# Optimization experiments

Hardware: AMD Instinct MI355X
Metric: run time of the kernel (lower is better)

The kernel has to match this reference:

```python
import jax, jax.numpy as jnp
import numpy as np

N, D, H, E, K = 4096, 512, 2048, 8, 2  # tokens, input_size, hidden_size, num_experts, top_k


def setup_inputs() -> dict:
    key = jax.random.key(0)
    ks = jax.random.split(key, 4)
    x = jax.random.normal(ks[0], (N, D), dtype=jnp.float32)
    # torch init: weights ~ N(0, 0.001), biases zero
    Wg = jax.random.normal(ks[1], (D, E), dtype=jnp.float32) * 0.001
    bg = jnp.zeros((E,), jnp.float32)
    W1 = jax.random.normal(ks[2], (E, D, H), dtype=jnp.float32) * 0.001
    b1 = jnp.zeros((E, H), jnp.float32)
    W2 = jax.random.normal(ks[3], (E, H, D), dtype=jnp.float32) * 0.001
    b2 = jnp.zeros((E, D), jnp.float32)
    return {"x": x, "Wg": Wg, "bg": bg, "W1": W1, "b1": b1, "W2": W2, "b2": b2}


def reference(x, Wg, bg, W1, b1, W2, b2):
    # Gating: softmax over experts
    gates = jax.nn.softmax(x @ Wg + bg, axis=-1)            # [N, E]
    top_w, top_i = jax.lax.top_k(gates, K)                  # [N, K]
    top_w = top_w / jnp.sum(top_w, axis=-1, keepdims=True)  # renormalize

    # Expert MLP (fc1 -> fc2, no nonlinearity per source). Vectorized across all
    # experts, then gather the top-k selected outputs per token.
    h1 = jnp.einsum('nd,edh->neh', x, W1) + b1              # [N, E, H]
    all_out = jnp.einsum('neh,ehd->ned', h1, W2) + b2       # [N, E, D]
    sel = jnp.take_along_axis(all_out, top_i[:, :, None], axis=1)  # [N, K, D]

    combined = jnp.einsum('nkd,nk->nd', sel, top_w)         # [N, D]

    # usage counts: scatter-add of (detached) top-k weights per expert
    usage = jnp.zeros((E,), x.dtype).at[top_i.reshape(-1)].add(
        jax.lax.stop_gradient(top_w).reshape(-1))
    return combined, usage
```

## Files before the change

### kernel.cpp

```cpp
#include <hip/hip_runtime.h>
#include <hip/hip_bf16.h>


#define N_TOK 4096
#define DIM   512
#define HID   2048
#define NEXP  8
#define TOTSLOT (2 * N_TOK)
#define MAXTILE 72

typedef __attribute__((ext_vector_type(8))) short short8;
typedef __attribute__((ext_vector_type(4))) float f32x4;

static __device__ __forceinline__ unsigned short f2bf(float f) {
    __hip_bfloat16 b = __float2bfloat16(f);
    return *reinterpret_cast<unsigned short*>(&b);
}
static __device__ __forceinline__ float bf2f(unsigned short u) {
    return __uint_as_float((unsigned)u << 16);
}

static __device__ __forceinline__ void load16_to_lds(const void* g, void* l) {
    __builtin_amdgcn_global_load_lds(
        (const __attribute__((address_space(1))) unsigned int*)g,
        (__attribute__((address_space(3))) unsigned int*)l, 16, 0, 0);
}

__global__ __launch_bounds__(256) void gating_kernel(
    const float* __restrict__ x, const float* __restrict__ Wg,
    const float* __restrict__ bg,
    int* __restrict__ cnt, int* __restrict__ te, float* __restrict__ tw,
    float* __restrict__ usage, unsigned short* __restrict__ Xb)
{
    __shared__ int   lcnt[NEXP];
    __shared__ float lus[NEXP];
    int tid = threadIdx.x;
    if (tid < NEXP) { lcnt[tid] = 0; lus[tid] = 0.f; }
    __syncthreads();

    int wave = tid >> 6;
    int lane = tid & 63;

    for (int t = 0; t < 4; ++t) {
        int n = blockIdx.x * 16 + wave * 4 + t;

        float acc[NEXP];
#pragma unroll
        for (int e = 0; e < NEXP; ++e) acc[e] = 0.f;

#pragma unroll
        for (int it = 0; it < DIM / 64; ++it) {
            int d = it * 64 + lane;
            float xv = x[n * DIM + d];
            Xb[n * DIM + d] = f2bf(xv);
            float4 wa = *(const float4*)&Wg[d * NEXP];
            float4 wb = *(const float4*)&Wg[d * NEXP + 4];
            acc[0] += xv * wa.x; acc[1] += xv * wa.y;
            acc[2] += xv * wa.z; acc[3] += xv * wa.w;
            acc[4] += xv * wb.x; acc[5] += xv * wb.y;
            acc[6] += xv * wb.z; acc[7] += xv * wb.w;
        }
#pragma unroll
        for (int m = 32; m >= 1; m >>= 1) {
#pragma unroll
            for (int e = 0; e < NEXP; ++e)
                acc[e] += __shfl_xor(acc[e], m, 64);
        }
        if (lane == 0) {
            float l[NEXP];
#pragma unroll
            for (int e = 0; e < NEXP; ++e) l[e] = acc[e] + bg[e];
            int i0 = 0;
#pragma unroll
            for (int e = 1; e < NEXP; ++e) if (l[e] > l[i0]) i0 = e;
            int i1 = (i0 == 0) ? 1 : 0;
#pragma unroll
            for (int e = 0; e < NEXP; ++e)
                if (e != i0 && l[e] > l[i1]) i1 = e;
            float w0 = 1.f / (1.f + expf(l[i1] - l[i0]));
            float w1 = 1.f - w0;
            te[n * 2] = i0; te[n * 2 + 1] = i1;
            tw[n * 2] = w0; tw[n * 2 + 1] = w1;
            atomicAdd(&lcnt[i0], 1);
            atomicAdd(&lcnt[i1], 1);
            atomicAdd(&lus[i0], w0);
            atomicAdd(&lus[i1], w1);
        }
    }
    __syncthreads();
    if (tid < NEXP) {
        if (lcnt[tid]) atomicAdd(&cnt[tid], lcnt[tid]);
        if (lus[tid] != 0.f) atomicAdd(&usage[tid], lus[tid]);
    }
}

__global__ void prefix_kernel(const int* __restrict__ cnt,
                              int* __restrict__ offs, int* __restrict__ fill,
                              unsigned short* __restrict__ tile_tab,
                              int* __restrict__ ntile)
{
    if (threadIdx.x == 0) {
        int s = 0, nt = 0;
        for (int e = 0; e < NEXP; ++e) {
            offs[e] = s; s += cnt[e];
            int t = (cnt[e] + 127) >> 7;
            for (int i = 0; i < t; ++i)
                tile_tab[nt++] = (unsigned short)((e << 8) | i);
        }
        *ntile = nt;
        for (int i = nt; i < MAXTILE; ++i) tile_tab[i] = 0;
    }
    if (threadIdx.x < NEXP) fill[threadIdx.x] = 0;
}

__global__ __launch_bounds__(256) void scatter_kernel(
    int* __restrict__ te, const float* __restrict__ tw,
    const int* __restrict__ offs, int* __restrict__ fill,
    int* __restrict__ btok, float* __restrict__ bwt)
{
    __shared__ int lcnt[NEXP];
    __shared__ int gbase[NEXP];
    int tid = threadIdx.x;
    if (tid < NEXP) lcnt[tid] = 0;
    __syncthreads();
    int n = blockIdx.x * 256 + tid;
    int e0 = te[n * 2], e1 = te[n * 2 + 1];
    int l0 = atomicAdd(&lcnt[e0], 1);
    int l1 = atomicAdd(&lcnt[e1], 1);
    __syncthreads();
    if (tid < NEXP) gbase[tid] = atomicAdd(&fill[tid], lcnt[tid]);
    __syncthreads();
    int s0 = offs[e0] + gbase[e0] + l0;
    int s1 = offs[e1] + gbase[e1] + l1;
    btok[s0] = n; bwt[s0] = tw[n * 2];
    btok[s1] = n; bwt[s1] = tw[n * 2 + 1];
    te[n * 2] = s0; te[n * 2 + 1] = s1;
}

__global__ __launch_bounds__(256) void transpose_cvt_kernel(
    const float* __restrict__ in, unsigned short* __restrict__ out,
    int R, int C)
{
    __shared__ unsigned short tile[64][65];
    int e = blockIdx.z;
    const float* src = in + (size_t)e * R * C;
    unsigned short* dst = out + (size_t)e * R * C;
    int r0 = blockIdx.x * 64, c0 = blockIdx.y * 64;
    int tid = threadIdx.x;
    int rr = tid >> 2, cb = (tid & 3) * 16;
#pragma unroll
    for (int i = 0; i < 4; ++i) {
        float4 v = *(const float4*)&src[(size_t)(r0 + rr) * C + c0 + cb + i * 4];
        tile[rr][cb + i * 4 + 0] = f2bf(v.x);
        tile[rr][cb + i * 4 + 1] = f2bf(v.y);
        tile[rr][cb + i * 4 + 2] = f2bf(v.z);
        tile[rr][cb + i * 4 + 3] = f2bf(v.w);
    }
    __syncthreads();
#pragma unroll
    for (int i = 0; i < 4; ++i) {
        ushort4 u;
        u.x = tile[cb + i * 4 + 0][rr];
        u.y = tile[cb + i * 4 + 1][rr];
        u.z = tile[cb + i * 4 + 2][rr];
        u.w = tile[cb + i * 4 + 3][rr];
        *(ushort4*)&dst[(size_t)(c0 + rr) * R + r0 + cb + i * 4] = u;
    }
}


__global__ __launch_bounds__(256) void gemm1_kernel(
    const unsigned short* __restrict__ Xb, const unsigned short* __restrict__ W1t,
    const float* __restrict__ b1, const int* __restrict__ cnt,
    const int* __restrict__ offs, const int* __restrict__ btok,
    const unsigned short* __restrict__ tile_tab, const int* __restrict__ ntile,
    unsigned short* __restrict__ H1)
{
    __shared__ __align__(16) unsigned short Ws[128 * 64];
    __shared__ __align__(16) unsigned short Xs[128 * 64];
    __shared__ int tok_s[128];

    int ti = blockIdx.x;
    if (ti >= *ntile) return;
    unsigned short tv = tile_tab[ti];
    int e = tv >> 8, tt = tv & 255, ht = blockIdx.y;
    int cn = cnt[e];
    int off_e = offs[e];
    int tid = threadIdx.x;

    if (tid < 128) {
        int lr = tt * 128 + tid;
        tok_s[tid] = (lr < cn) ? btok[off_e + lr] : 0;
    }
    __syncthreads();

    int wave = tid >> 6, lane = tid & 63;
    int mbase = (wave >> 1) * 64, nbase = (wave & 1) * 64;
    int quad = lane >> 4, lcol = lane & 15;
    f32x4 acc[4][4];
#pragma unroll
    for (int mi = 0; mi < 4; ++mi)
#pragma unroll
        for (int ni = 0; ni < 4; ++ni)
            acc[mi][ni] = (f32x4){0.f, 0.f, 0.f, 0.f};

    int Rb = tid >> 3, pc = tid & 7;
    const unsigned short* Wsrc = W1t + ((size_t)e * HID + ht * 128) * DIM;

    for (int k0 = 0; k0 < DIM; k0 += 64) {
#pragma unroll
        for (int p = 0; p < 4; ++p) {
            int R = Rb + p * 32;
            int c = pc ^ (R & 7);
            load16_to_lds(&Wsrc[(size_t)R * DIM + k0 + c * 8], &Ws[R * 64 + pc * 8]);
            load16_to_lds(&Xb[(size_t)tok_s[R] * DIM + k0 + c * 8], &Xs[R * 64 + pc * 8]);
        }
        __syncthreads();
#pragma unroll
        for (int h = 0; h < 2; ++h) {
            int cs = ((h * 4 + quad) ^ (lcol & 7)) * 8;
            short8 a[4], b[4];
#pragma unroll
            for (int i = 0; i < 4; ++i) {
                a[i] = *(const short8*)&Ws[(mbase + i * 16 + lcol) * 64 + cs];
                b[i] = *(const short8*)&Xs[(nbase + i * 16 + lcol) * 64 + cs];
            }
#pragma unroll
            for (int mi = 0; mi < 4; ++mi)
#pragma unroll
                for (int ni = 0; ni < 4; ++ni)
                    acc[mi][ni] = __builtin_amdgcn_mfma_f32_16x16x32_bf16(
                        a[mi], b[ni], acc[mi][ni], 0, 0, 0);
        }
        __syncthreads();
    }

    float4 bv[4];
#pragma unroll
    for (int mi = 0; mi < 4; ++mi)
        bv[mi] = *(const float4*)&b1[e * HID + ht * 128 + mbase + mi * 16 + quad * 4];
#pragma unroll
    for (int ni = 0; ni < 4; ++ni) {
        int tn = tt * 128 + nbase + ni * 16 + lcol;
        if (tn >= cn) continue;
        size_t srow = (size_t)(off_e + tn) * HID + ht * 128;
#pragma unroll
        for (int mi = 0; mi < 4; ++mi) {
            int hh = mbase + mi * 16 + quad * 4;
            ushort4 u;
            u.x = f2bf(acc[mi][ni][0] + bv[mi].x);
            u.y = f2bf(acc[mi][ni][1] + bv[mi].y);
            u.z = f2bf(acc[mi][ni][2] + bv[mi].z);
            u.w = f2bf(acc[mi][ni][3] + bv[mi].w);
            *(ushort4*)&H1[srow + hh] = u;
        }
    }
}

#define KSPLIT 2
#define KCH (HID / KSPLIT)

__global__ __launch_bounds__(256) void gemm2_kernel(
    const unsigned short* __restrict__ H1, const unsigned short* __restrict__ W2t,
    const float* __restrict__ b2, const int* __restrict__ cnt,
    const int* __restrict__ offs, const int* __restrict__ btok,
    const float* __restrict__ bwt,
    const unsigned short* __restrict__ tile_tab, const int* __restrict__ ntile,
    unsigned short* __restrict__ O)
{
    __shared__ __align__(16) unsigned short Ws[128 * 64];
    __shared__ __align__(16) unsigned short Hs[128 * 64];
    __shared__ float wt_s[128];

    int ti = blockIdx.x;
    if (ti >= *ntile) return;
    unsigned short tv = tile_tab[ti];
    int e = tv >> 8, tt = tv & 255, dt = blockIdx.y, kz = blockIdx.z;
    int cn = cnt[e];
    int off_e = offs[e];
    int sb = off_e + tt * 128;
    int tid = threadIdx.x;

    if (tid < 128) {
        int lr = tt * 128 + tid;
        wt_s[tid] = (lr < cn) ? bwt[off_e + lr] : 0.f;
    }
    __syncthreads();

    int wave = tid >> 6, lane = tid & 63;
    int mbase = (wave >> 1) * 64, nbase = (wave & 1) * 64;
    int quad = lane >> 4, lcol = lane & 15;
    f32x4 acc[4][4];
#pragma unroll
    for (int mi = 0; mi < 4; ++mi)
#pragma unroll
        for (int ni = 0; ni < 4; ++ni)
            acc[mi][ni] = (f32x4){0.f, 0.f, 0.f, 0.f};

    int Rb = tid >> 3, pc = tid & 7;
    const unsigned short* Wsrc = W2t + ((size_t)e * DIM + dt * 128) * HID;

    for (int k0 = kz * KCH; k0 < (kz + 1) * KCH; k0 += 64) {
#pragma unroll
        for (int p = 0; p < 4; ++p) {
            int R = Rb + p * 32;
            int c = pc ^ (R & 7);
            int sr = sb + R; if (sr > TOTSLOT - 1) sr = TOTSLOT - 1;
            load16_to_lds(&Wsrc[(size_t)R * HID + k0 + c * 8], &Ws[R * 64 + pc * 8]);
            load16_to_lds(&H1[(size_t)sr * HID + k0 + c * 8], &Hs[R * 64 + pc * 8]);
        }
        __syncthreads();
#pragma unroll
        for (int h = 0; h < 2; ++h) {
            int cs = ((h * 4 + quad) ^ (lcol & 7)) * 8;
            short8 a[4], b[4];
#pragma unroll
            for (int i = 0; i < 4; ++i) {
                a[i] = *(const short8*)&Hs[(mbase + i * 16 + lcol) * 64 + cs];
                b[i] = *(const short8*)&Ws[(nbase + i * 16 + lcol) * 64 + cs];
            }
#pragma unroll
            for (int mi = 0; mi < 4; ++mi)
#pragma unroll
                for (int ni = 0; ni < 4; ++ni)
                    acc[mi][ni] = __builtin_amdgcn_mfma_f32_16x16x32_bf16(
                        a[mi], b[ni], acc[mi][ni], 0, 0, 0);
        }
        __syncthreads();
    }

    unsigned short* Oe = O + ((size_t)kz * TOTSLOT + sb) * DIM + dt * 128;
#pragma unroll
    for (int ni = 0; ni < 4; ++ni) {
        int dl = nbase + ni * 16 + lcol;
        float bv = (kz == 0) ? b2[e * DIM + dt * 128 + dl] : 0.f;
#pragma unroll
        for (int mi = 0; mi < 4; ++mi) {
            int rl = mbase + mi * 16 + quad * 4;
#pragma unroll
            for (int r = 0; r < 4; ++r) {
                int sl = rl + r;
                if (tt * 128 + sl < cn)
                    Oe[(size_t)sl * DIM + dl] = f2bf(wt_s[sl] * (acc[mi][ni][r] + bv));
            }
        }
    }
}

__global__ __launch_bounds__(256) void combine_kernel(
    const unsigned short* __restrict__ O, const int* __restrict__ sidx,
    float* __restrict__ out)
{
    int tid = threadIdx.x;
    int n = blockIdx.x * 2 + (tid >> 7);
    int dd = (tid & 127) * 4;
    int s0 = sidx[n * 2], s1 = sidx[n * 2 + 1];
    ushort4 a = *(const ushort4*)&O[(size_t)s0 * DIM + dd];
    ushort4 b = *(const ushort4*)&O[((size_t)TOTSLOT + s0) * DIM + dd];
    ushort4 c = *(const ushort4*)&O[(size_t)s1 * DIM + dd];
    ushort4 d = *(const ushort4*)&O[((size_t)TOTSLOT + s1) * DIM + dd];
    float4 o;
    o.x = bf2f(a.x) + bf2f(b.x) + bf2f(c.x) + bf2f(d.x);
    o.y = bf2f(a.y) + bf2f(b.y) + bf2f(c.y) + bf2f(d.y);
    o.z = bf2f(a.z) + bf2f(b.z) + bf2f(c.z) + bf2f(d.z);
    o.w = bf2f(a.w) + bf2f(b.w) + bf2f(c.w) + bf2f(d.w);
    *(float4*)&out[(size_t)n * DIM + dd] = o;
}

#define TN 16
#define HC 256
#define NCHUNK (HID / HC)

__global__ __launch_bounds__(256) void gating_fb_kernel(
    const float* __restrict__ x, const float* __restrict__ Wg,
    const float* __restrict__ bg,
    int* __restrict__ cnt, int* __restrict__ btok, float* __restrict__ bwt,
    float* __restrict__ usage)
{
    int wave = threadIdx.x >> 6;
    int lane = threadIdx.x & 63;
    int n = blockIdx.x * 4 + wave;
    float acc[NEXP];
#pragma unroll
    for (int e = 0; e < NEXP; ++e) acc[e] = 0.f;
    for (int d = lane; d < DIM; d += 64) {
        float xv = x[n * DIM + d];
        float4 wa = *(const float4*)&Wg[d * NEXP];
        float4 wb = *(const float4*)&Wg[d * NEXP + 4];
        acc[0] += xv * wa.x; acc[1] += xv * wa.y;
        acc[2] += xv * wa.z; acc[3] += xv * wa.w;
        acc[4] += xv * wb.x; acc[5] += xv * wb.y;
        acc[6] += xv * wb.z; acc[7] += xv * wb.w;
    }
#pragma unroll
    for (int m = 32; m >= 1; m >>= 1)
#pragma unroll
        for (int e = 0; e < NEXP; ++e)
            acc[e] += __shfl_xor(acc[e], m, 64);
    if (lane == 0) {
        float l[NEXP];
#pragma unroll
        for (int e = 0; e < NEXP; ++e) l[e] = acc[e] + bg[e];
        int i0 = 0;
#pragma unroll
        for (int e = 1; e < NEXP; ++e) if (l[e] > l[i0]) i0 = e;
        int i1 = (i0 == 0) ? 1 : 0;
#pragma unroll
        for (int e = 0; e < NEXP; ++e)
            if (e != i0 && l[e] > l[i1]) i1 = e;
        float w0 = 1.f / (1.f + expf(l[i1] - l[i0]));
        float w1 = 1.f - w0;
        int p0 = atomicAdd(&cnt[i0], 1);
        btok[i0 * N_TOK + p0] = n; bwt[i0 * N_TOK + p0] = w0;
        int p1 = atomicAdd(&cnt[i1], 1);
        btok[i1 * N_TOK + p1] = n; bwt[i1 * N_TOK + p1] = w1;
        atomicAdd(&usage[i0], w0);
        atomicAdd(&usage[i1], w1);
    }
}

__global__ __launch_bounds__(256) void expert_fb_kernel(
    const float* __restrict__ x, const float* __restrict__ W1,
    const float* __restrict__ b1, const float* __restrict__ W2,
    const float* __restrict__ b2, const int* __restrict__ cnt,
    const int* __restrict__ btok, const float* __restrict__ bwt,
    float* __restrict__ out)
{
    __shared__ float xs[TN][DIM];
    __shared__ float h1s[TN][HC];
    __shared__ int   tok_s[TN];
    __shared__ float wt_s[TN];
    int e = blockIdx.x >> 8;
    int tile = blockIdx.x & 255;
    int cn = cnt[e];
    int n0 = tile * TN;
    if (n0 >= cn) return;
    int nt = min(TN, cn - n0);
    int tid = threadIdx.x;
    if (tid < TN) {
        if (tid < nt) { tok_s[tid] = btok[e * N_TOK + n0 + tid]; wt_s[tid] = bwt[e * N_TOK + n0 + tid]; }
        else          { tok_s[tid] = 0; wt_s[tid] = 0.f; }
    }
    __syncthreads();
    for (int idx = tid; idx < TN * DIM; idx += 256) {
        int t = idx >> 9, d = idx & 511;
        xs[t][d] = (t < nt) ? x[tok_s[t] * DIM + d] : 0.f;
    }
    const float* W1e = W1 + (size_t)e * DIM * HID;
    const float* W2e = W2 + (size_t)e * HID * DIM;
    int tg = tid >> 6, lane = tid & 63;
    float oacc[4][8];
    {
        float4 ba = *(const float4*)&b2[e * DIM + lane * 8];
        float4 bb = *(const float4*)&b2[e * DIM + lane * 8 + 4];
#pragma unroll
        for (int ti = 0; ti < 4; ++ti) {
            oacc[ti][0] = ba.x; oacc[ti][1] = ba.y; oacc[ti][2] = ba.z; oacc[ti][3] = ba.w;
            oacc[ti][4] = bb.x; oacc[ti][5] = bb.y; oacc[ti][6] = bb.z; oacc[ti][7] = bb.w;
        }
    }
    __syncthreads();
    for (int ch = 0; ch < NCHUNK; ++ch) {
        int h0 = ch * HC;
        float f[4][4];
        {
            float4 b1v = *(const float4*)&b1[e * HID + h0 + lane * 4];
#pragma unroll
            for (int ti = 0; ti < 4; ++ti) {
                f[ti][0] = b1v.x; f[ti][1] = b1v.y; f[ti][2] = b1v.z; f[ti][3] = b1v.w;
            }
        }
        for (int d = 0; d < DIM; ++d) {
            float4 w1v = *(const float4*)&W1e[(size_t)d * HID + h0 + lane * 4];
#pragma unroll
            for (int ti = 0; ti < 4; ++ti) {
                float xv = xs[tg + 4 * ti][d];
                f[ti][0] += xv * w1v.x; f[ti][1] += xv * w1v.y;
                f[ti][2] += xv * w1v.z; f[ti][3] += xv * w1v.w;
            }
        }
        __syncthreads();
#pragma unroll
        for (int ti = 0; ti < 4; ++ti)
            *(float4*)&h1s[tg + 4 * ti][lane * 4] = make_float4(f[ti][0], f[ti][1], f[ti][2], f[ti][3]);
        __syncthreads();
        for (int j = 0; j < HC; ++j) {
            const float* w2row = &W2e[(size_t)(h0 + j) * DIM + lane * 8];
            float4 wa = *(const float4*)w2row;
            float4 wb = *(const float4*)(w2row + 4);
#pragma unroll
            for (int ti = 0; ti < 4; ++ti) {
                float hv = h1s[tg + 4 * ti][j];
                oacc[ti][0] += hv * wa.x; oacc[ti][1] += hv * wa.y;
                oacc[ti][2] += hv * wa.z; oacc[ti][3] += hv * wa.w;
                oacc[ti][4] += hv * wb.x; oacc[ti][5] += hv * wb.y;
                oacc[ti][6] += hv * wb.z; oacc[ti][7] += hv * wb.w;
            }
        }
    }
#pragma unroll
    for (int ti = 0; ti < 4; ++ti) {
        int t = tg + 4 * ti;
        if (t < nt) {
            float w = wt_s[t];
            float* o = &out[(size_t)tok_s[t] * DIM + lane * 8];
#pragma unroll
            for (int c = 0; c < 8; ++c)
                atomicAdd(&o[c], w * oacc[ti][c]);
        }
    }
}

extern "C" void kernel_launch(void* const* d_in, const int* in_sizes, int n_in,
                              void* d_out, int out_size, void* d_ws, size_t ws_size,
                              hipStream_t stream) {
    const float* x  = (const float*)d_in[0];
    const float* Wg = (const float*)d_in[1];
    const float* bg = (const float*)d_in[2];
    const float* W1 = (const float*)d_in[3];
    const float* b1 = (const float*)d_in[4];
    const float* W2 = (const float*)d_in[5];
    const float* b2 = (const float*)d_in[6];

    float* out   = (float*)d_out;
    float* usage = out + (size_t)N_TOK * DIM;

    char* ws = (char*)d_ws;
    int*   cnt  = (int*)(ws + 0);
    int*   fill = (int*)(ws + 32);
    int*   offs = (int*)(ws + 64);
    unsigned short* tile_tab = (unsigned short*)(ws + 96);
    int*   ntile = (int*)(ws + 240);
    int*   te   = (int*)(ws + 256);
    float* tw   = (float*)(ws + 33024);
    int*   btok = (int*)(ws + 65792);
    float* bwt  = (float*)(ws + 98560);
    unsigned short* Xb  = (unsigned short*)(ws + 131328);
    unsigned short* W1t = (unsigned short*)(ws + 4325632);
    unsigned short* O   = W1t;
    unsigned short* W2t = (unsigned short*)(ws + 21102848);
    unsigned short* H1  = (unsigned short*)(ws + 37880064);
    const size_t WS_NEED = 71434496ULL;

    if (ws_size >= WS_NEED) {
        hipMemsetAsync(cnt, 0, 32, stream);
        hipMemsetAsync(usage, 0, NEXP * sizeof(float), stream);
        transpose_cvt_kernel<<<dim3(DIM / 64, HID / 64, NEXP), 256, 0, stream>>>(W1, W1t, DIM, HID);
        transpose_cvt_kernel<<<dim3(HID / 64, DIM / 64, NEXP), 256, 0, stream>>>(W2, W2t, HID, DIM);
        gating_kernel<<<N_TOK / 16, 256, 0, stream>>>(x, Wg, bg, cnt, te, tw, usage, Xb);
        prefix_kernel<<<1, 64, 0, stream>>>(cnt, offs, fill, tile_tab, ntile);
        scatter_kernel<<<N_TOK / 256, 256, 0, stream>>>(te, tw, offs, fill, btok, bwt);
        gemm1_kernel<<<dim3(MAXTILE, HID / 128), 256, 0, stream>>>(
            Xb, W1t, b1, cnt, offs, btok, tile_tab, ntile, H1);
        gemm2_kernel<<<dim3(MAXTILE, DIM / 128, KSPLIT), 256, 0, stream>>>(
            H1, W2t, b2, cnt, offs, btok, bwt, tile_tab, ntile, O);
        combine_kernel<<<N_TOK / 2, 256, 0, stream>>>(O, te, out);
    } else {
        int*   fcnt  = (int*)d_ws;
        int*   fbtok = (int*)((char*)d_ws + 256);
        float* fbwt  = (float*)((char*)d_ws + 256 + (size_t)NEXP * N_TOK * sizeof(int));
        hipMemsetAsync(d_out, 0, (size_t)(N_TOK * DIM + NEXP) * sizeof(float), stream);
        hipMemsetAsync(d_ws, 0, 256, stream);
        gating_fb_kernel<<<N_TOK / 4, 256, 0, stream>>>(x, Wg, bg, fcnt, fbtok, fbwt, usage);
        expert_fb_kernel<<<NEXP * (N_TOK / TN), 256, 0, stream>>>(
            x, W1, b1, W2, b2, fcnt, fbtok, fbwt, out);
    }
}
```

Baseline: 224.7 us.

## Double-buffer LDS tiles in both expert GEMMs and remap tile block order

```diff
diff --git a/kernel.cpp b/kernel.cpp
--- a/kernel.cpp
+++ b/kernel.cpp
@@ -176,11 +176,12 @@
     const unsigned short* __restrict__ tile_tab, const int* __restrict__ ntile,
     unsigned short* __restrict__ H1)
 {
-    __shared__ __align__(16) unsigned short Ws[128 * 64];
-    __shared__ __align__(16) unsigned short Xs[128 * 64];
+    __shared__ __align__(16) unsigned short Ws[2][128 * 64];
+    __shared__ __align__(16) unsigned short Xs[2][128 * 64];
     __shared__ int tok_s[128];
 
-    int ti = blockIdx.x;
+    int bx = blockIdx.x;
+    int ti = (bx & 7) * (MAXTILE / 8) + (bx >> 3);
     if (ti >= *ntile) return;
     unsigned short tv = tile_tab[ti];
     int e = tv >> 8, tt = tv & 255, ht = blockIdx.y;
@@ -207,23 +208,31 @@
     int Rb = tid >> 3, pc = tid & 7;
     const unsigned short* Wsrc = W1t + ((size_t)e * HID + ht * 128) * DIM;
 
-    for (int k0 = 0; k0 < DIM; k0 += 64) {
+    auto stage = [&](int buf, int k0) {
 #pragma unroll
         for (int p = 0; p < 4; ++p) {
             int R = Rb + p * 32;
             int c = pc ^ (R & 7);
-            load16_to_lds(&Wsrc[(size_t)R * DIM + k0 + c * 8], &Ws[R * 64 + pc * 8]);
-            load16_to_lds(&Xb[(size_t)tok_s[R] * DIM + k0 + c * 8], &Xs[R * 64 + pc * 8]);
-        }
-        __syncthreads();
+            load16_to_lds(&Wsrc[(size_t)R * DIM + k0 + c * 8], &Ws[buf][R * 64 + pc * 8]);
+            load16_to_lds(&Xb[(size_t)tok_s[R] * DIM + k0 + c * 8], &Xs[buf][R * 64 + pc * 8]);
+        }
+    };
+
+    stage(0, 0);
+    __syncthreads();
+
+    const int NT = DIM / 64;
+    for (int t = 0; t < NT; ++t) {
+        int cur = t & 1;
+        if (t + 1 < NT) stage(cur ^ 1, (t + 1) * 64);
 #pragma unroll
         for (int h = 0; h < 2; ++h) {
             int cs = ((h * 4 + quad) ^ (lcol & 7)) * 8;
             short8 a[4], b[4];
 #pragma unroll
             for (int i = 0; i < 4; ++i) {
-                a[i] = *(const short8*)&Ws[(mbase + i * 16 + lcol) * 64 + cs];
-                b[i] = *(const short8*)&Xs[(nbase + i * 16 + lcol) * 64 + cs];
+                a[i] = *(const short8*)&Ws[cur][(mbase + i * 16 + lcol) * 64 + cs];
+                b[i] = *(const short8*)&Xs[cur][(nbase + i * 16 + lcol) * 64 + cs];
             }
 #pragma unroll
             for (int mi = 0; mi < 4; ++mi)
@@ -268,11 +277,12 @@
     const unsigned short* __restrict__ tile_tab, const int* __restrict__ ntile,
     unsigned short* __restrict__ O)
 {
-    __shared__ __align__(16) unsigned short Ws[128 * 64];
-    __shared__ __align__(16) unsigned short Hs[128 * 64];
+    __shared__ __align__(16) unsigned short Ws[2][128 * 64];
+    __shared__ __align__(16) unsigned short Hs[2][128 * 64];
     __shared__ float wt_s[128];
 
-    int ti = blockIdx.x;
+    int bx = blockIdx.x;
+    int ti = (bx & 7) * (MAXTILE / 8) + (bx >> 3);
     if (ti >= *ntile) return;
     unsigned short tv = tile_tab[ti];
     int e = tv >> 8, tt = tv & 255, dt = blockIdx.y, kz = blockIdx.z;
@@ -300,24 +310,32 @@
     int Rb = tid >> 3, pc = tid & 7;
     const unsigned short* Wsrc = W2t + ((size_t)e * DIM + dt * 128) * HID;
 
-    for (int k0 = kz * KCH; k0 < (kz + 1) * KCH; k0 += 64) {
+    auto stage = [&](int buf, int k0) {
 #pragma unroll
         for (int p = 0; p < 4; ++p) {
             int R = Rb + p * 32;
             int c = pc ^ (R & 7);
             int sr = sb + R; if (sr > TOTSLOT - 1) sr = TOTSLOT - 1;
-            load16_to_lds(&Wsrc[(size_t)R * HID + k0 + c * 8], &Ws[R * 64 + pc * 8]);
-            load16_to_lds(&H1[(size_t)sr * HID + k0 + c * 8], &Hs[R * 64 + pc * 8]);
-        }
-        __syncthreads();
+            load16_to_lds(&Wsrc[(size_t)R * HID + k0 + c * 8], &Ws[buf][R * 64 + pc * 8]);
+            load16_to_lds(&H1[(size_t)sr * HID + k0 + c * 8], &Hs[buf][R * 64 + pc * 8]);
+        }
+    };
+
+    stage(0, kz * KCH);
+    __syncthreads();
+
+    const int NT = KCH / 64;
+    for (int t = 0; t < NT; ++t) {
+        int cur = t & 1;
+        if (t + 1 < NT) stage(cur ^ 1, kz * KCH + (t + 1) * 64);
 #pragma unroll
         for (int h = 0; h < 2; ++h) {
             int cs = ((h * 4 + quad) ^ (lcol & 7)) * 8;
             short8 a[4], b[4];
 #pragma unroll
             for (int i = 0; i < 4; ++i) {
-                a[i] = *(const short8*)&Hs[(mbase + i * 16 + lcol) * 64 + cs];
-                b[i] = *(const short8*)&Ws[(nbase + i * 16 + lcol) * 64 + cs];
+                a[i] = *(const short8*)&Hs[cur][(mbase + i * 16 + lcol) * 64 + cs];
+                b[i] = *(const short8*)&Ws[cur][(nbase + i * 16 + lcol) * 64 + cs];
             }
 #pragma unroll
             for (int mi = 0; mi < 4; ++mi)
```

Result: slower. 239.6 us (+6.6%).

## Halve gemm2 token tile and swizzle expert tiles across XCDs

Applied to the files above, without the earlier changes.

```diff
diff --git a/kernel.cpp b/kernel.cpp
--- a/kernel.cpp
+++ b/kernel.cpp
@@ -7,7 +7,8 @@
 #define HID   2048
 #define NEXP  8
 #define TOTSLOT (2 * N_TOK)
-#define MAXTILE 72
+#define M1TILE 72
+#define M2TILE 144
 
 typedef __attribute__((ext_vector_type(8))) short short8;
 typedef __attribute__((ext_vector_type(4))) float f32x4;
@@ -96,19 +97,18 @@
 
 __global__ void prefix_kernel(const int* __restrict__ cnt,
                               int* __restrict__ offs, int* __restrict__ fill,
-                              unsigned short* __restrict__ tile_tab,
+                              int* __restrict__ tb128, int* __restrict__ tb64,
                               int* __restrict__ ntile)
 {
     if (threadIdx.x == 0) {
-        int s = 0, nt = 0;
+        int s = 0, a = 0, b = 0;
         for (int e = 0; e < NEXP; ++e) {
             offs[e] = s; s += cnt[e];
-            int t = (cnt[e] + 127) >> 7;
-            for (int i = 0; i < t; ++i)
-                tile_tab[nt++] = (unsigned short)((e << 8) | i);
-        }
-        *ntile = nt;
-        for (int i = nt; i < MAXTILE; ++i) tile_tab[i] = 0;
+            tb128[e] = a; a += (cnt[e] + 127) >> 7;
+            tb64[e]  = b; b += (cnt[e] + 63) >> 6;
+        }
+        tb128[NEXP] = a; tb64[NEXP] = b;
+        ntile[0] = a; ntile[1] = b;
     }
     if (threadIdx.x < NEXP) fill[threadIdx.x] = 0;
 }
@@ -173,17 +173,21 @@
     const unsigned short* __restrict__ Xb, const unsigned short* __restrict__ W1t,
     const float* __restrict__ b1, const int* __restrict__ cnt,
     const int* __restrict__ offs, const int* __restrict__ btok,
-    const unsigned short* __restrict__ tile_tab, const int* __restrict__ ntile,
+    const int* __restrict__ tb128, const int* __restrict__ ntile,
     unsigned short* __restrict__ H1)
 {
     __shared__ __align__(16) unsigned short Ws[128 * 64];
     __shared__ __align__(16) unsigned short Xs[128 * 64];
     __shared__ int tok_s[128];
 
-    int ti = blockIdx.x;
-    if (ti >= *ntile) return;
-    unsigned short tv = tile_tab[ti];
-    int e = tv >> 8, tt = tv & 255, ht = blockIdx.y;
+    int bx = blockIdx.x;
+    int ti = (bx & 7) * (M1TILE / 8) + (bx >> 3);
+    if (ti >= ntile[0]) return;
+    int e = 0;
+#pragma unroll
+    for (int k = 1; k < NEXP; ++k) if (ti >= tb128[k]) e = k;
+    int tt = ti - tb128[e];
+    int ht = blockIdx.y;
     int cn = cnt[e];
     int off_e = offs[e];
     int tid = threadIdx.x;
@@ -263,38 +267,40 @@
 __global__ __launch_bounds__(256) void gemm2_kernel(
     const unsigned short* __restrict__ H1, const unsigned short* __restrict__ W2t,
     const float* __restrict__ b2, const int* __restrict__ cnt,
-    const int* __restrict__ offs, const int* __restrict__ btok,
-    const float* __restrict__ bwt,
-    const unsigned short* __restrict__ tile_tab, const int* __restrict__ ntile,
+    const int* __restrict__ offs, const float* __restrict__ bwt,
+    const int* __restrict__ tb64, const int* __restrict__ ntile,
     unsigned short* __restrict__ O)
 {
     __shared__ __align__(16) unsigned short Ws[128 * 64];
-    __shared__ __align__(16) unsigned short Hs[128 * 64];
-    __shared__ float wt_s[128];
-
-    int ti = blockIdx.x;
-    if (ti >= *ntile) return;
-    unsigned short tv = tile_tab[ti];
-    int e = tv >> 8, tt = tv & 255, dt = blockIdx.y, kz = blockIdx.z;
+    __shared__ __align__(16) unsigned short Hs[64 * 64];
+    __shared__ float wt_s[64];
+
+    int bx = blockIdx.x;
+    int ti = (bx & 7) * (M2TILE / 8) + (bx >> 3);
+    if (ti >= ntile[1]) return;
+    int e = 0;
+#pragma unroll
+    for (int k = 1; k < NEXP; ++k) if (ti >= tb64[k]) e = k;
+    int tt = ti - tb64[e];
+    int dt = blockIdx.y, kz = blockIdx.z;
     int cn = cnt[e];
     int off_e = offs[e];
-    int sb = off_e + tt * 128;
-    int tid = threadIdx.x;
-
-    if (tid < 128) {
-        int lr = tt * 128 + tid;
+    int sb = off_e + tt * 64;
+    int tid = threadIdx.x;
+
+    if (tid < 64) {
+        int lr = tt * 64 + tid;
         wt_s[tid] = (lr < cn) ? bwt[off_e + lr] : 0.f;
     }
-    __syncthreads();
 
     int wave = tid >> 6, lane = tid & 63;
-    int mbase = (wave >> 1) * 64, nbase = (wave & 1) * 64;
+    int nbase = wave * 32;
     int quad = lane >> 4, lcol = lane & 15;
-    f32x4 acc[4][4];
+    f32x4 acc[4][2];
 #pragma unroll
     for (int mi = 0; mi < 4; ++mi)
 #pragma unroll
-        for (int ni = 0; ni < 4; ++ni)
+        for (int ni = 0; ni < 2; ++ni)
             acc[mi][ni] = (f32x4){0.f, 0.f, 0.f, 0.f};
 
     int Rb = tid >> 3, pc = tid & 7;
@@ -305,24 +311,30 @@
         for (int p = 0; p < 4; ++p) {
             int R = Rb + p * 32;
             int c = pc ^ (R & 7);
+            load16_to_lds(&Wsrc[(size_t)R * HID + k0 + c * 8], &Ws[R * 64 + pc * 8]);
+        }
+#pragma unroll
+        for (int p = 0; p < 2; ++p) {
+            int R = Rb + p * 32;
+            int c = pc ^ (R & 7);
             int sr = sb + R; if (sr > TOTSLOT - 1) sr = TOTSLOT - 1;
-            load16_to_lds(&Wsrc[(size_t)R * HID + k0 + c * 8], &Ws[R * 64 + pc * 8]);
             load16_to_lds(&H1[(size_t)sr * HID + k0 + c * 8], &Hs[R * 64 + pc * 8]);
         }
         __syncthreads();
 #pragma unroll
         for (int h = 0; h < 2; ++h) {
             int cs = ((h * 4 + quad) ^ (lcol & 7)) * 8;
-            short8 a[4], b[4];
-#pragma unroll
-            for (int i = 0; i < 4; ++i) {
-                a[i] = *(const short8*)&Hs[(mbase + i * 16 + lcol) * 64 + cs];
+            short8 a[4], b[2];
+#pragma unroll
+            for (int i = 0; i < 4; ++i)
+                a[i] = *(const short8*)&Hs[(i * 16 + lcol) * 64 + cs];
+#pragma unroll
+            for (int i = 0; i < 2; ++i)
                 b[i] = *(const short8*)&Ws[(nbase + i * 16 + lcol) * 64 + cs];
-            }
 #pragma unroll
             for (int mi = 0; mi < 4; ++mi)
 #pragma unroll
-                for (int ni = 0; ni < 4; ++ni)
+                for (int ni = 0; ni < 2; ++ni)
                     acc[mi][ni] = __builtin_amdgcn_mfma_f32_16x16x32_bf16(
                         a[mi], b[ni], acc[mi][ni], 0, 0, 0);
         }
@@ -331,16 +343,16 @@
 
     unsigned short* Oe = O + ((size_t)kz * TOTSLOT + sb) * DIM + dt * 128;
 #pragma unroll
-    for (int ni = 0; ni < 4; ++ni) {
+    for (int ni = 0; ni < 2; ++ni) {
         int dl = nbase + ni * 16 + lcol;
         float bv = (kz == 0) ? b2[e * DIM + dt * 128 + dl] : 0.f;
 #pragma unroll
         for (int mi = 0; mi < 4; ++mi) {
-            int rl = mbase + mi * 16 + quad * 4;
+            int rl = mi * 16 + quad * 4;
 #pragma unroll
             for (int r = 0; r < 4; ++r) {
                 int sl = rl + r;
-                if (tt * 128 + sl < cn)
+                if (tt * 64 + sl < cn)
                     Oe[(size_t)sl * DIM + dl] = f2bf(wt_s[sl] * (acc[mi][ni][r] + bv));
             }
         }
@@ -526,11 +538,12 @@
     float* usage = out + (size_t)N_TOK * DIM;
 
     char* ws = (char*)d_ws;
-    int*   cnt  = (int*)(ws + 0);
-    int*   fill = (int*)(ws + 32);
-    int*   offs = (int*)(ws + 64);
-    unsigned short* tile_tab = (unsigned short*)(ws + 96);
-    int*   ntile = (int*)(ws + 240);
+    int*   cnt   = (int*)(ws + 0);
+    int*   fill  = (int*)(ws + 32);
+    int*   offs  = (int*)(ws + 64);
+    int*   tb128 = (int*)(ws + 96);
+    int*   tb64  = (int*)(ws + 132);
+    int*   ntile = (int*)(ws + 168);
     int*   te   = (int*)(ws + 256);
     float* tw   = (float*)(ws + 33024);
     int*   btok = (int*)(ws + 65792);
@@ -548,12 +561,12 @@
         transpose_cvt_kernel<<<dim3(DIM / 64, HID / 64, NEXP), 256, 0, stream>>>(W1, W1t, DIM, HID);
         transpose_cvt_kernel<<<dim3(HID / 64, DIM / 64, NEXP), 256, 0, stream>>>(W2, W2t, HID, DIM);
         gating_kernel<<<N_TOK / 16, 256, 0, stream>>>(x, Wg, bg, cnt, te, tw, usage, Xb);
-        prefix_kernel<<<1, 64, 0, stream>>>(cnt, offs, fill, tile_tab, ntile);
+        prefix_kernel<<<1, 64, 0, stream>>>(cnt, offs, fill, tb128, tb64, ntile);
         scatter_kernel<<<N_TOK / 256, 256, 0, stream>>>(te, tw, offs, fill, btok, bwt);
-        gemm1_kernel<<<dim3(MAXTILE, HID / 128), 256, 0, stream>>>(
-            Xb, W1t, b1, cnt, offs, btok, tile_tab, ntile, H1);
-        gemm2_kernel<<<dim3(MAXTILE, DIM / 128, KSPLIT), 256, 0, stream>>>(
-            H1, W2t, b2, cnt, offs, btok, bwt, tile_tab, ntile, O);
+        gemm1_kernel<<<dim3(M1TILE, HID / 128), 256, 0, stream>>>(
+            Xb, W1t, b1, cnt, offs, btok, tb128, ntile, H1);
+        gemm2_kernel<<<dim3(M2TILE, DIM / 128, KSPLIT), 256, 0, stream>>>(
+            H1, W2t, b2, cnt, offs, bwt, tb64, ntile, O);
         combine_kernel<<<N_TOK / 2, 256, 0, stream>>>(O, te, out);
     } else {
         int*   fcnt  = (int*)d_ws;
```

Result: faster. 212.0 us (-5.7%).
